# Performance work log

Hardware: AMD Instinct MI355X
Metric: run time of the kernel (lower is better)

Reference implementation:

```python
import jax, jax.numpy as jnp
import numpy as np

DECAY = 0.99
EPS = 1e-05


def setup_inputs() -> dict:
    key = jax.random.key(0)
    k1, k2 = jax.random.split(key)
    B, T, D, K = 16, 4096, 256, 1024
    z = jax.random.normal(k1, (B, T, D), dtype=jnp.float32)
    embedding = jax.random.normal(k2, (D, K), dtype=jnp.float32)
    cluster_size = jnp.zeros((K,), dtype=jnp.float32)
    embedding_mean = embedding.copy()  # torch init: embedding.clone()
    return {"z": z, "embedding": embedding, "cluster_size": cluster_size,
            "embedding_mean": embedding_mean}


def reference(z, embedding, cluster_size, embedding_mean):
    """Training-mode forward of CodebookEMA (proj=False).

    z:              [B, T, D]
    embedding:      [D, K] codebook buffer
    cluster_size:   [K]    EMA cluster counts
    embedding_mean: [D, K] EMA cluster sums
    Returns (z_q, commitment_loss, codebook_loss, code,
             new_embedding, new_cluster_size, new_embedding_mean).
    """
    B, T, D = z.shape
    K = embedding.shape[1]
    z_flat = z.reshape(B * T, D)

    # squared-distance quantization: ||z||^2 - 2 z.E + ||e||^2  -> [BT, K]
    dist = ((z_flat * z_flat).sum(1, keepdims=True)
            - 2.0 * (z_flat @ embedding)
            + (embedding * embedding).sum(0)[None, :])
    idx = jnp.argmin(dist, axis=1)              # [BT]
    code = idx.reshape(B, T)

    # EMA codebook update (no one-hot materialization; use segment sums)
    counts = jax.ops.segment_sum(jnp.ones_like(idx, dtype=z.dtype), idx,
                                 num_segments=K)               # [K]
    emb_sum = jax.ops.segment_sum(z_flat, idx, num_segments=K).T  # [D, K]
    new_cluster_size = cluster_size * DECAY + (1.0 - DECAY) * counts
    new_embedding_mean = embedding_mean * DECAY + (1.0 - DECAY) * emb_sum
    n = new_cluster_size.sum()
    cs_norm = (new_cluster_size + EPS) / (n + K * EPS) * n     # Laplace-smoothed
    new_embedding = new_embedding_mean / cs_norm[None, :]      # [D, K]

    # dequantize with the *updated* codebook (as in the torch control flow)
    z_q = new_embedding.T[code]                                # [B, T, D]

    commitment_loss = ((jax.lax.stop_gradient(z_q) - z) ** 2).mean(axis=(1, 2))
    codebook_loss = jnp.zeros((B,), dtype=z.dtype)
    z_q = z + jax.lax.stop_gradient(z_q - z)  # straight-through estimator
    return (z_q, commitment_loss, codebook_loss, code,
            new_embedding, new_cluster_size, new_embedding_mean)
```

## Files before the change

### kernel.cpp

```cpp
#include <hip/hip_runtime.h>
#include <cfloat>
#include <climits>
#include <cstdint>

#define B_ 16
#define T_ 4096
#define D_ 256
#define K_ 1024
#define BT_ 65536
#define DECAYF 0.99f
#define OMDECAYF 0.01f
#define EPSF 1e-5f
#define TAUGAP 0.125f
#define CHUNK 32
#define GROUP 16
#define RMARGIN 0.01f

typedef float f32x4 __attribute__((ext_vector_type(4)));
typedef _Float16 f16x8 __attribute__((ext_vector_type(8)));

__device__ __forceinline__ void gload16(const void* g, void* l) {
    __builtin_amdgcn_global_load_lds(
        (const __attribute__((address_space(1))) void*)g,
        (__attribute__((address_space(3))) void*)l, 16, 0, 0);
}

__global__ void k_prep(const float* __restrict__ z, const float* __restrict__ E,
                       _Float16* __restrict__ zf, _Float16* __restrict__ EfT,
                       float* __restrict__ enorm, double* __restrict__ enorm64,
                       int* __restrict__ counts, int* __restrict__ nflag,
                       float* __restrict__ out_closs, float* __restrict__ out_cbl,
                       float* __restrict__ emb_sum) {
    int b = blockIdx.x;
    if (b < 8192) {
        int base = (b * 256 + threadIdx.x) * 8;
        float4 v0 = *(const float4*)(z + base);
        float4 v1 = *(const float4*)(z + base + 4);
        f16x8 h;
        h[0] = (_Float16)v0.x; h[1] = (_Float16)v0.y;
        h[2] = (_Float16)v0.z; h[3] = (_Float16)v0.w;
        h[4] = (_Float16)v1.x; h[5] = (_Float16)v1.y;
        h[6] = (_Float16)v1.z; h[7] = (_Float16)v1.w;
        *(f16x8*)(zf + base) = h;
    } else {
        __shared__ double rd[256];
        int n = b - 8192, d = threadIdx.x;
        float v = E[(size_t)d * K_ + n];
        EfT[(size_t)n * 256 + d] = (_Float16)v;
        rd[d] = (double)v * (double)v;
        __syncthreads();
        for (int st = 128; st > 0; st >>= 1) {
            if (d < st) rd[d] += rd[d + st];
            __syncthreads();
        }
        if (d == 0) { enorm[n] = (float)rd[0]; enorm64[n] = rd[0]; }
        emb_sum[(size_t)n * 256 + d] = 0.f;
        if (n < 4) counts[n * 256 + d] = 0;
        if (n == 4) {
            if (d < 16) out_closs[d] = 0.f;
            else if (d < 32) out_cbl[d - 16] = 0.f;
            else if (d == 32) *nflag = 0;
        }
    }
}

__global__ __launch_bounds__(512, 2) void k_argmin_mfma(
    const _Float16* __restrict__ zf, const _Float16* __restrict__ EfT,
    const float* __restrict__ enorm, int* __restrict__ code,
    int* __restrict__ flags, int* __restrict__ nflag, int* __restrict__ counts) {
    __shared__ _Float16 Ab[2][128 * 32];
    __shared__ _Float16 Bb[2][256 * 32];
    __shared__ float mg_d1[512];
    __shared__ int   mg_i1[512];
    __shared__ float mg_d2[512];

    const int t = threadIdx.x;
    const int row0 = blockIdx.x * 128;
    const int l = t & 63, wid = t >> 6;
    const int wr = wid >> 2, wc = wid & 3;
    const int lr = l & 15, lk = l >> 4;

    const int arow = t >> 2,          ablk = (t & 3) ^ ((arow >> 1) & 3);
    const int brow0 = t >> 2,         bblk0 = (t & 3) ^ ((brow0 >> 1) & 3);
    const int brow1 = (t + 512) >> 2, bblk1 = ((t + 512) & 3) ^ ((brow1 >> 1) & 3);

#define STAGE(it_, buf_) do {                                                       \
        int nc_ = (it_) >> 3; int kb_ = ((it_) & 7) * 32;                            \
        gload16(zf + (size_t)(row0 + arow) * 256 + kb_ + ablk * 8,                   \
                &Ab[buf_][(t & ~63) * 8]);                                           \
        gload16(EfT + (size_t)(nc_ * 256 + brow0) * 256 + kb_ + bblk0 * 8,           \
                &Bb[buf_][(t & ~63) * 8]);                                           \
        gload16(EfT + (size_t)(nc_ * 256 + brow1) * 256 + kb_ + bblk1 * 8,           \
                &Bb[buf_][((t + 512) & ~63) * 8]);                                   \
    } while (0)

    STAGE(0, 0);

    float D1[4][4], D2[4][4];
    int   I1[4][4];
    #pragma unroll
    for (int m = 0; m < 4; ++m)
        #pragma unroll
        for (int r = 0; r < 4; ++r) {
            D1[m][r] = FLT_MAX; D2[m][r] = FLT_MAX; I1[m][r] = 0x7fffffff;
        }

    f32x4 acc[4][4];
    for (int it = 0; it < 32; ++it) {
        if ((it & 7) == 0) {
            #pragma unroll
            for (int m = 0; m < 4; ++m)
                #pragma unroll
                for (int n = 0; n < 4; ++n) acc[m][n] = (f32x4){0.f, 0.f, 0.f, 0.f};
        }
        __syncthreads();
        if (it + 1 < 32) STAGE(it + 1, (it + 1) & 1);
        const _Float16* Abuf = Ab[it & 1];
        const _Float16* Bbuf = Bb[it & 1];
        f16x8 a[4], b[4];
        #pragma unroll
        for (int m = 0; m < 4; ++m) {
            int row = wr * 64 + m * 16 + lr;
            a[m] = *(const f16x8*)&Abuf[row * 32 + ((lk ^ ((row >> 1) & 3)) * 8)];
        }
        #pragma unroll
        for (int n = 0; n < 4; ++n) {
            int nn = wc * 64 + n * 16 + lr;
            b[n] = *(const f16x8*)&Bbuf[nn * 32 + ((lk ^ ((nn >> 1) & 3)) * 8)];
        }
        #pragma unroll
        for (int m = 0; m < 4; ++m)
            #pragma unroll
            for (int n = 0; n < 4; ++n)
                acc[m][n] = __builtin_amdgcn_mfma_f32_16x16x32_f16(
                    a[m], b[n], acc[m][n], 0, 0, 0);

        if ((it & 7) == 7) {
            int nc = it >> 3;
            float en[4];
            #pragma unroll
            for (int n = 0; n < 4; ++n)
                en[n] = enorm[nc * 256 + wc * 64 + n * 16 + lr];
            #pragma unroll
            for (int m = 0; m < 4; ++m)
                #pragma unroll
                for (int r = 0; r < 4; ++r)
                    #pragma unroll
                    for (int n = 0; n < 4; ++n) {
                        float dist = en[n] - 2.0f * acc[m][n][r];
                        int cg = nc * 256 + wc * 64 + n * 16 + lr;
                        if (dist < D1[m][r]) {
                            D2[m][r] = D1[m][r]; D1[m][r] = dist; I1[m][r] = cg;
                        } else D2[m][r] = fminf(D2[m][r], dist);
                    }
        }
    }
#undef STAGE

    #pragma unroll
    for (int m = 0; m < 4; ++m)
        #pragma unroll
        for (int r = 0; r < 4; ++r) {
            float d1 = D1[m][r], d2 = D2[m][r];
            int i1 = I1[m][r];
            #pragma unroll
            for (int mask = 1; mask < 16; mask <<= 1) {
                float pd1 = __shfl_xor(d1, mask);
                int   pi1 = __shfl_xor(i1, mask);
                float pd2 = __shfl_xor(d2, mask);
                if (pd1 < d1 || (pd1 == d1 && pi1 < i1)) {
                    d2 = fminf(d1, pd2); d1 = pd1; i1 = pi1;
                } else d2 = fminf(d2, pd1);
            }
            if (lr == 0) {
                int row = wr * 64 + m * 16 + lk * 4 + r;
                mg_d1[row * 4 + wc] = d1;
                mg_i1[row * 4 + wc] = i1;
                mg_d2[row * 4 + wc] = d2;
            }
        }
    __syncthreads();
    if (t < 128) {
        float b1 = FLT_MAX, b2 = FLT_MAX;
        int bi = 0x7fffffff;
        #pragma unroll
        for (int c = 0; c < 4; ++c) {
            float pd1 = mg_d1[t * 4 + c];
            int   pi1 = mg_i1[t * 4 + c];
            float pd2 = mg_d2[t * 4 + c];
            if (pd1 < b1 || (pd1 == b1 && pi1 < bi)) {
                b2 = fminf(b1, pd2); b1 = pd1; bi = pi1;
            } else b2 = fminf(b2, pd1);
        }
        code[row0 + t] = bi;
        atomicAdd(&counts[bi], 1);
        if (b2 - b1 < TAUGAP) {
            int pos = atomicAdd(nflag, 1);
            flags[pos] = row0 + t;
        }
    }
}

__global__ __launch_bounds__(256) void k_fixup(
    const float* __restrict__ z, const float* __restrict__ E,
    const float* __restrict__ enorm, const double* __restrict__ enorm64,
    const int* __restrict__ nflag, const int* __restrict__ flags,
    int* __restrict__ code, int* __restrict__ counts) {
    __shared__ float  zrows[GROUP][256];
    __shared__ int    rowid[GROUP];
    __shared__ float  bw[GROUP][4];
    __shared__ float  bestAll[GROUP];
    __shared__ int    ccnt[GROUP];
    __shared__ int    cand[GROUP][16];
    __shared__ double cdist[GROUP][16];

    const int t = threadIdx.x, w = t >> 6, l = t & 63;
    const int n = *nflag;
    const int ngroups = (n + GROUP - 1) / GROUP;

    for (int g = blockIdx.x; g < ngroups; g += gridDim.x) {
        __syncthreads();
        if (t < GROUP) {
            int idx = g * GROUP + t;
            rowid[t] = (idx < n) ? flags[idx] : -1;
            ccnt[t] = 0;
        }
        __syncthreads();
        {
            int i = t >> 4, s = t & 15;
            int r = rowid[i];
            const float* src = z + (size_t)(r < 0 ? 0 : r) * D_ + s * 16;
            float4 a0 = *(const float4*)(src + 0);
            float4 a1 = *(const float4*)(src + 4);
            float4 a2 = *(const float4*)(src + 8);
            float4 a3 = *(const float4*)(src + 12);
            *(float4*)&zrows[i][s * 16 + 0]  = a0;
            *(float4*)&zrows[i][s * 16 + 4]  = a1;
            *(float4*)&zrows[i][s * 16 + 8]  = a2;
            *(float4*)&zrows[i][s * 16 + 12] = a3;
        }
        __syncthreads();

        float acc[GROUP][4];
        #pragma unroll
        for (int i = 0; i < GROUP; ++i) {
            acc[i][0] = 0.f; acc[i][1] = 0.f; acc[i][2] = 0.f; acc[i][3] = 0.f;
        }
        const float* Ecol = E + 4 * t;
        for (int d = 0; d < D_; ++d) {
            float4 ev = *(const float4*)(Ecol + (size_t)d * K_);
            #pragma unroll
            for (int i = 0; i < GROUP; ++i) {
                float zd = zrows[i][d];
                acc[i][0] = fmaf(zd, ev.x, acc[i][0]);
                acc[i][1] = fmaf(zd, ev.y, acc[i][1]);
                acc[i][2] = fmaf(zd, ev.z, acc[i][2]);
                acc[i][3] = fmaf(zd, ev.w, acc[i][3]);
            }
        }
        float en0 = enorm[4 * t], en1 = enorm[4 * t + 1];
        float en2 = enorm[4 * t + 2], en3 = enorm[4 * t + 3];
        #pragma unroll
        for (int i = 0; i < GROUP; ++i) {
            acc[i][0] = en0 - 2.f * acc[i][0];
            acc[i][1] = en1 - 2.f * acc[i][1];
            acc[i][2] = en2 - 2.f * acc[i][2];
            acc[i][3] = en3 - 2.f * acc[i][3];
        }
        #pragma unroll
        for (int i = 0; i < GROUP; ++i) {
            float b = fminf(fminf(acc[i][0], acc[i][1]), fminf(acc[i][2], acc[i][3]));
            #pragma unroll
            for (int m = 1; m < 64; m <<= 1) b = fminf(b, __shfl_xor(b, m));
            if (l == 0) bw[i][w] = b;
        }
        __syncthreads();
        if (t < GROUP)
            bestAll[t] = fminf(fminf(bw[t][0], bw[t][1]), fminf(bw[t][2], bw[t][3]));
        __syncthreads();
        #pragma unroll
        for (int i = 0; i < GROUP; ++i) {
            float thr = bestAll[i] + RMARGIN;
            #pragma unroll
            for (int j = 0; j < 4; ++j) {
                if (acc[i][j] <= thr) {
                    int slot = atomicAdd(&ccnt[i], 1);
                    if (slot < 16) cand[i][slot] = 4 * t + j;
                }
            }
        }
        __syncthreads();
        for (int p = w; p < GROUP * 16; p += 4) {
            int i = p >> 4, s = p & 15;
            int cn = ccnt[i];
            if (rowid[i] < 0 || cn < 2 || s >= (cn < 16 ? cn : 16)) continue;
            int c = cand[i][s];
            double dot = 0.0;
            #pragma unroll
            for (int q = 0; q < 4; ++q) {
                int d = l * 4 + q;
                dot = fma((double)zrows[i][d], (double)E[(size_t)d * K_ + c], dot);
            }
            #pragma unroll
            for (int m = 1; m < 64; m <<= 1) dot += __shfl_xor(dot, m);
            if (l == 0) cdist[i][s] = enorm64[c] - 2.0 * dot;
        }
        __syncthreads();
        if (t < GROUP) {
            int r = rowid[t];
            if (r >= 0) {
                int cn = ccnt[t]; if (cn > 16) cn = 16;
                int newc;
                if (cn <= 1) {
                    newc = cand[t][0];
                } else {
                    double bd = DBL_MAX; int bi = INT_MAX;
                    for (int s = 0; s < cn; ++s) {
                        double dv = cdist[t][s]; int ci = cand[t][s];
                        if (dv < bd || (dv == bd && ci < bi)) { bd = dv; bi = ci; }
                    }
                    newc = bi;
                }
                int oldc = code[r];
                if (newc != oldc) {
                    code[r] = newc;
                    atomicSub(&counts[oldc], 1);
                    atomicAdd(&counts[newc], 1);
                }
            }
        }
    }
}

__global__ void k_scan(const int* __restrict__ counts, const float* __restrict__ cs,
                       int* __restrict__ offsets, int* __restrict__ cursor,
                       float* __restrict__ out_newcs, float* __restrict__ csnorm,
                       int* __restrict__ work, int* __restrict__ nwork) {
    __shared__ int   s[K_];
    __shared__ int   c[K_];
    __shared__ float red[K_];
    int t = threadIdx.x;
    int v = counts[t];
    int nch = (v + CHUNK - 1) / CHUNK;
    s[t] = v;
    c[t] = nch;
    float ncs = cs[t] * DECAYF + OMDECAYF * (float)v;
    out_newcs[t] = ncs;
    red[t] = ncs;
    __syncthreads();
    for (int d = 1; d < K_; d <<= 1) {
        int x = (t >= d) ? s[t - d] : 0;
        int y = (t >= d) ? c[t - d] : 0;
        __syncthreads();
        s[t] += x; c[t] += y;
        __syncthreads();
    }
    offsets[t] = s[t] - v;
    cursor[t]  = s[t] - v;
    if (t == K_ - 1) { offsets[K_] = s[t]; *nwork = c[t]; }
    int wbase = c[t] - nch;
    for (int j = 0; j < nch; ++j) work[wbase + j] = (t << 16) | j;
    for (int st = 512; st > 0; st >>= 1) {
        if (t < st) red[t] += red[t + st];
        __syncthreads();
    }
    float nsum = red[0];
    csnorm[t] = (ncs + EPSF) / (nsum + (float)K_ * EPSF) * nsum;
}

__global__ void k_sortidx(const int* __restrict__ code, int* __restrict__ cursor,
                          int* __restrict__ sorted) {
    int r = blockIdx.x * 256 + threadIdx.x;
    int cc = code[r];
    int pos = atomicAdd(&cursor[cc], 1);
    sorted[pos] = r;
}

__global__ void k_segsum(const float* __restrict__ z, const int* __restrict__ sorted,
                         const int* __restrict__ offsets, const int* __restrict__ work,
                         const int* __restrict__ nwork, float* __restrict__ emb_sum) {
    int NW = *nwork;
    int d = threadIdx.x;
    for (int i = blockIdx.x; i < NW; i += gridDim.x) {
        int wk = work[i];
        int k = wk >> 16, j = wk & 0xffff;
        int beg = offsets[k] + j * CHUNK;
        int end = min(beg + CHUNK, offsets[k + 1]);
        float s = 0.f;
        int idx = beg;
        for (; idx + 4 <= end; idx += 4) {
            int r0 = sorted[idx], r1 = sorted[idx + 1];
            int r2 = sorted[idx + 2], r3 = sorted[idx + 3];
            float v0 = z[(size_t)r0 * D_ + d];
            float v1 = z[(size_t)r1 * D_ + d];
            float v2 = z[(size_t)r2 * D_ + d];
            float v3 = z[(size_t)r3 * D_ + d];
            s += (v0 + v1) + (v2 + v3);
        }
        for (; idx < end; ++idx) s += z[(size_t)sorted[idx] * D_ + d];
        atomicAdd(&emb_sum[(size_t)k * D_ + d], s);
    }
}

__global__ void k_emb(const float* __restrict__ EM, const float* __restrict__ emb_sum,
                      const float* __restrict__ csnorm,
                      float* __restrict__ out_newemb, float* __restrict__ out_newem,
                      float* __restrict__ newembT) {
    int tid = blockIdx.x * 256 + threadIdx.x;
    int k = tid >> 8, d = tid & 255;
    float em  = EM[(size_t)d * K_ + k];
    float nem = em * DECAYF + OMDECAYF * emb_sum[tid];
    float nq  = nem / csnorm[k];
    out_newem [(size_t)d * K_ + k] = nem;
    out_newemb[(size_t)d * K_ + k] = nq;
    newembT[tid] = nq;
}

__global__ __launch_bounds__(256) void k_gather(
    const float* __restrict__ z, const int* __restrict__ code,
    const float* __restrict__ newembT,
    float* __restrict__ out_zq, float* __restrict__ out_code,
    float* __restrict__ out_closs) {
    __shared__ double wsum[4];
    const int w = threadIdx.x >> 6, l = threadIdx.x & 63;
    const int base = blockIdx.x * 32 + w * 8;
    double acc = 0.0;
    #pragma unroll
    for (int it = 0; it < 2; ++it) {
        const int r0 = base + it * 4;
        int i0 = code[r0], i1 = code[r0 + 1], i2 = code[r0 + 2], i3 = code[r0 + 3];
        float4 z0 = *(const float4*)(z + (size_t)(r0    ) * D_ + l * 4);
        float4 z1 = *(const float4*)(z + (size_t)(r0 + 1) * D_ + l * 4);
        float4 z2 = *(const float4*)(z + (size_t)(r0 + 2) * D_ + l * 4);
        float4 z3 = *(const float4*)(z + (size_t)(r0 + 3) * D_ + l * 4);
        float4 e0 = *(const float4*)(newembT + (size_t)i0 * D_ + l * 4);
        float4 e1 = *(const float4*)(newembT + (size_t)i1 * D_ + l * 4);
        float4 e2 = *(const float4*)(newembT + (size_t)i2 * D_ + l * 4);
        float4 e3 = *(const float4*)(newembT + (size_t)i3 * D_ + l * 4);
        *(float4*)(out_zq + (size_t)(r0    ) * D_ + l * 4) = e0;
        *(float4*)(out_zq + (size_t)(r0 + 1) * D_ + l * 4) = e1;
        *(float4*)(out_zq + (size_t)(r0 + 2) * D_ + l * 4) = e2;
        *(float4*)(out_zq + (size_t)(r0 + 3) * D_ + l * 4) = e3;
        if (l < 4) out_code[r0 + l] = (float)(l == 0 ? i0 : l == 1 ? i1 : l == 2 ? i2 : i3);
        float dx, dy, dz2, dw2;
        dx = e0.x - z0.x; dy = e0.y - z0.y; dz2 = e0.z - z0.z; dw2 = e0.w - z0.w;
        acc += (double)dx * dx + (double)dy * dy + (double)dz2 * dz2 + (double)dw2 * dw2;
        dx = e1.x - z1.x; dy = e1.y - z1.y; dz2 = e1.z - z1.z; dw2 = e1.w - z1.w;
        acc += (double)dx * dx + (double)dy * dy + (double)dz2 * dz2 + (double)dw2 * dw2;
        dx = e2.x - z2.x; dy = e2.y - z2.y; dz2 = e2.z - z2.z; dw2 = e2.w - z2.w;
        acc += (double)dx * dx + (double)dy * dy + (double)dz2 * dz2 + (double)dw2 * dw2;
        dx = e3.x - z3.x; dy = e3.y - z3.y; dz2 = e3.z - z3.z; dw2 = e3.w - z3.w;
        acc += (double)dx * dx + (double)dy * dy + (double)dz2 * dz2 + (double)dw2 * dw2;
    }
    #pragma unroll
    for (int off = 32; off > 0; off >>= 1) acc += __shfl_down(acc, off);
    if (l == 0) wsum[w] = acc;
    __syncthreads();
    if (threadIdx.x == 0) {
        float v = (float)((wsum[0] + wsum[1] + wsum[2] + wsum[3]) *
                          (1.0 / ((double)T_ * (double)D_)));
        atomicAdd(&out_closs[blockIdx.x >> 7], v);
    }
}

extern "C" void kernel_launch(void* const* d_in, const int* in_sizes, int n_in,
                              void* d_out, int out_size, void* d_ws, size_t ws_size,
                              hipStream_t stream) {
    (void)in_sizes; (void)n_in; (void)out_size; (void)ws_size;
    const float* z  = (const float*)d_in[0];
    const float* E  = (const float*)d_in[1];
    const float* cs = (const float*)d_in[2];
    const float* EM = (const float*)d_in[3];

    float* out       = (float*)d_out;
    float* out_zq    = out;
    float* out_closs = out + 16777216;
    float* out_cbl   = out_closs + 16;
    float* out_code  = out_cbl + 16;
    float* out_nemb  = out_code + 65536;
    float* out_ncs   = out_nemb + 262144;
    float* out_nem   = out_ncs + 1024;

    _Float16* zf = (_Float16*)out_zq;

    char* w = (char*)d_ws;
    int*      counts  = (int*)(w + 0);
    int*      nflag   = (int*)(w + 4096);
    int*      offsets = (int*)(w + 4160);
    int*      cursor  = (int*)(w + 8320);
    float*    enorm   = (float*)(w + 12416);
    int*      code_i  = (int*)(w + 16512);
    int*      flags   = (int*)(w + 278656);
    float*    csnorm  = (float*)(w + 540800);
    float*    newembT = (float*)(w + 544896);
    _Float16* EfT     = (_Float16*)(w + 1593472);
    int*      sorted  = (int*)(w + 2117760);
    float*    emb_sum = (float*)(w + 2379904);
    int*      work    = (int*)(w + 3428480);
    int*      nwork   = (int*)(w + 3444864);
    double*   enorm64 = (double*)(w + 3444928);

    k_prep       <<<9216, 256, 0, stream>>>(z, E, zf, EfT, enorm, enorm64, counts,
                                            nflag, out_closs, out_cbl, emb_sum);
    k_argmin_mfma<<<BT_ / 128, 512, 0, stream>>>(zf, EfT, enorm, code_i, flags,
                                                 nflag, counts);
    k_fixup      <<<256, 256, 0, stream>>>(z, E, enorm, enorm64, nflag, flags,
                                           code_i, counts);
    k_scan       <<<1, K_, 0, stream>>>(counts, cs, offsets, cursor, out_ncs, csnorm,
                                        work, nwork);
    k_sortidx    <<<BT_ / 256, 256, 0, stream>>>(code_i, cursor, sorted);
    k_segsum     <<<2048, 256, 0, stream>>>(z, sorted, offsets, work, nwork, emb_sum);
    k_emb        <<<(K_ * D_) / 256, 256, 0, stream>>>(EM, emb_sum, csnorm,
                                                       out_nemb, out_nem, newembT);
    k_gather     <<<BT_ / 32, 256, 0, stream>>>(z, code_i, newembT, out_zq, out_code,
                                                out_closs);
}
```

Baseline: 291.2 us.

## Raise argmin occupancy, reuse LDS for merge, unroll segsum and gather loads

The argmin kernel's launch bounds move from 2 to 6 waves-per-EU hint, and its merge scratch arrays now alias the A tile buffer after a barrier instead of taking extra LDS. Both changes aim to fit more blocks per CU. The segment-sum inner loop is unrolled to 8 rows to put more loads in flight. The gather kernel issues all 8 rows' loads up front rather than in two batches. The tighter register budget risks spills in the MFMA argmin kernel, and the gather and segsum unrolls raise register pressure.

```diff
diff --git a/kernel.cpp b/kernel.cpp
--- a/kernel.cpp
+++ b/kernel.cpp
@@ -64,15 +64,12 @@
     }
 }
 
-__global__ __launch_bounds__(512, 2) void k_argmin_mfma(
+__global__ __launch_bounds__(512, 6) void k_argmin_mfma(
     const _Float16* __restrict__ zf, const _Float16* __restrict__ EfT,
     const float* __restrict__ enorm, int* __restrict__ code,
     int* __restrict__ flags, int* __restrict__ nflag, int* __restrict__ counts) {
     __shared__ _Float16 Ab[2][128 * 32];
     __shared__ _Float16 Bb[2][256 * 32];
-    __shared__ float mg_d1[512];
-    __shared__ int   mg_i1[512];
-    __shared__ float mg_d2[512];
 
     const int t = threadIdx.x;
     const int row0 = blockIdx.x * 128;
@@ -156,6 +153,11 @@
         }
     }
 #undef STAGE
+
+    __syncthreads();
+    float* mg_d1 = (float*)&Ab[0][0];
+    int*   mg_i1 = (int*)(mg_d1 + 512);
+    float* mg_d2 = (float*)(mg_i1 + 512);
 
     #pragma unroll
     for (int m = 0; m < 4; ++m)
@@ -388,14 +390,20 @@
         int end = min(beg + CHUNK, offsets[k + 1]);
         float s = 0.f;
         int idx = beg;
-        for (; idx + 4 <= end; idx += 4) {
-            int r0 = sorted[idx], r1 = sorted[idx + 1];
+        for (; idx + 8 <= end; idx += 8) {
+            int r0 = sorted[idx],     r1 = sorted[idx + 1];
             int r2 = sorted[idx + 2], r3 = sorted[idx + 3];
+            int r4 = sorted[idx + 4], r5 = sorted[idx + 5];
+            int r6 = sorted[idx + 6], r7 = sorted[idx + 7];
             float v0 = z[(size_t)r0 * D_ + d];
             float v1 = z[(size_t)r1 * D_ + d];
             float v2 = z[(size_t)r2 * D_ + d];
             float v3 = z[(size_t)r3 * D_ + d];
-            s += (v0 + v1) + (v2 + v3);
+            float v4 = z[(size_t)r4 * D_ + d];
+            float v5 = z[(size_t)r5 * D_ + d];
+            float v6 = z[(size_t)r6 * D_ + d];
+            float v7 = z[(size_t)r7 * D_ + d];
+            s += ((v0 + v1) + (v2 + v3)) + ((v4 + v5) + (v6 + v7));
         }
         for (; idx < end; ++idx) s += z[(size_t)sorted[idx] * D_ + d];
         atomicAdd(&emb_sum[(size_t)k * D_ + d], s);
@@ -424,34 +432,56 @@
     __shared__ double wsum[4];
     const int w = threadIdx.x >> 6, l = threadIdx.x & 63;
     const int base = blockIdx.x * 32 + w * 8;
+    int i0 = code[base],     i1 = code[base + 1], i2 = code[base + 2], i3 = code[base + 3];
+    int i4 = code[base + 4], i5 = code[base + 5], i6 = code[base + 6], i7 = code[base + 7];
+    float4 z0 = *(const float4*)(z + (size_t)(base    ) * D_ + l * 4);
+    float4 z1 = *(const float4*)(z + (size_t)(base + 1) * D_ + l * 4);
+    float4 z2 = *(const float4*)(z + (size_t)(base + 2) * D_ + l * 4);
+    float4 z3 = *(const float4*)(z + (size_t)(base + 3) * D_ + l * 4);
+    float4 z4 = *(const float4*)(z + (size_t)(base + 4) * D_ + l * 4);
+    float4 z5 = *(const float4*)(z + (size_t)(base + 5) * D_ + l * 4);
+    float4 z6 = *(const float4*)(z + (size_t)(base + 6) * D_ + l * 4);
+    float4 z7 = *(const float4*)(z + (size_t)(base + 7) * D_ + l * 4);
+    float4 e0 = *(const float4*)(newembT + (size_t)i0 * D_ + l * 4);
+    float4 e1 = *(const float4*)(newembT + (size_t)i1 * D_ + l * 4);
+    float4 e2 = *(const float4*)(newembT + (size_t)i2 * D_ + l * 4);
+    float4 e3 = *(const float4*)(newembT + (size_t)i3 * D_ + l * 4);
+    float4 e4 = *(const float4*)(newembT + (size_t)i4 * D_ + l * 4);
+    float4 e5 = *(const float4*)(newembT + (size_t)i5 * D_ + l * 4);
+    float4 e6 = *(const float4*)(newembT + (size_t)i6 * D_ + l * 4);
+    float4 e7 = *(const float4*)(newembT + (size_t)i7 * D_ + l * 4);
+    *(float4*)(out_zq + (size_t)(base    ) * D_ + l * 4) = e0;
+    *(float4*)(out_zq + (size_t)(base + 1) * D_ + l * 4) = e1;
+    *(float4*)(out_zq + (size_t)(base + 2) * D_ + l * 4) = e2;
+    *(float4*)(out_zq + (size_t)(base + 3) * D_ + l * 4) = e3;
+    *(float4*)(out_zq + (size_t)(base + 4) * D_ + l * 4) = e4;
+    *(float4*)(out_zq + (size_t)(base + 5) * D_ + l * 4) = e5;
+    *(float4*)(out_zq + (size_t)(base + 6) * D_ + l * 4) = e6;
+    *(float4*)(out_zq + (size_t)(base + 7) * D_ + l * 4) = e7;
+    if (l == 0) {
+        out_code[base]     = (float)i0; out_code[base + 1] = (float)i1;
+        out_code[base + 2] = (float)i2; out_code[base + 3] = (float)i3;
+        out_code[base + 4] = (float)i4; out_code[base + 5] = (float)i5;
+        out_code[base + 6] = (float)i6; out_code[base + 7] = (float)i7;
+    }
     double acc = 0.0;
-    #pragma unroll
-    for (int it = 0; it < 2; ++it) {
-        const int r0 = base + it * 4;
-        int i0 = code[r0], i1 = code[r0 + 1], i2 = code[r0 + 2], i3 = code[r0 + 3];
-        float4 z0 = *(const float4*)(z + (size_t)(r0    ) * D_ + l * 4);
-        float4 z1 = *(const float4*)(z + (size_t)(r0 + 1) * D_ + l * 4);
-        float4 z2 = *(const float4*)(z + (size_t)(r0 + 2) * D_ + l * 4);
-        float4 z3 = *(const float4*)(z + (size_t)(r0 + 3) * D_ + l * 4);
-        float4 e0 = *(const float4*)(newembT + (size_t)i0 * D_ + l * 4);
-        float4 e1 = *(const float4*)(newembT + (size_t)i1 * D_ + l * 4);
-        float4 e2 = *(const float4*)(newembT + (size_t)i2 * D_ + l * 4);
-        float4 e3 = *(const float4*)(newembT + (size_t)i3 * D_ + l * 4);
-        *(float4*)(out_zq + (size_t)(r0    ) * D_ + l * 4) = e0;
-        *(float4*)(out_zq + (size_t)(r0 + 1) * D_ + l * 4) = e1;
-        *(float4*)(out_zq + (size_t)(r0 + 2) * D_ + l * 4) = e2;
-        *(float4*)(out_zq + (size_t)(r0 + 3) * D_ + l * 4) = e3;
-        if (l < 4) out_code[r0 + l] = (float)(l == 0 ? i0 : l == 1 ? i1 : l == 2 ? i2 : i3);
-        float dx, dy, dz2, dw2;
-        dx = e0.x - z0.x; dy = e0.y - z0.y; dz2 = e0.z - z0.z; dw2 = e0.w - z0.w;
-        acc += (double)dx * dx + (double)dy * dy + (double)dz2 * dz2 + (double)dw2 * dw2;
-        dx = e1.x - z1.x; dy = e1.y - z1.y; dz2 = e1.z - z1.z; dw2 = e1.w - z1.w;
-        acc += (double)dx * dx + (double)dy * dy + (double)dz2 * dz2 + (double)dw2 * dw2;
-        dx = e2.x - z2.x; dy = e2.y - z2.y; dz2 = e2.z - z2.z; dw2 = e2.w - z2.w;
-        acc += (double)dx * dx + (double)dy * dy + (double)dz2 * dz2 + (double)dw2 * dw2;
-        dx = e3.x - z3.x; dy = e3.y - z3.y; dz2 = e3.z - z3.z; dw2 = e3.w - z3.w;
-        acc += (double)dx * dx + (double)dy * dy + (double)dz2 * dz2 + (double)dw2 * dw2;
-    }
+    float dx, dy, dz2, dw2;
+    dx = e0.x - z0.x; dy = e0.y - z0.y; dz2 = e0.z - z0.z; dw2 = e0.w - z0.w;
+    acc += (double)dx * dx + (double)dy * dy + (double)dz2 * dz2 + (double)dw2 * dw2;
+    dx = e1.x - z1.x; dy = e1.y - z1.y; dz2 = e1.z - z1.z; dw2 = e1.w - z1.w;
+    acc += (double)dx * dx + (double)dy * dy + (double)dz2 * dz2 + (double)dw2 * dw2;
+    dx = e2.x - z2.x; dy = e2.y - z2.y; dz2 = e2.z - z2.z; dw2 = e2.w - z2.w;
+    acc += (double)dx * dx + (double)dy * dy + (double)dz2 * dz2 + (double)dw2 * dw2;
+    dx = e3.x - z3.x; dy = e3.y - z3.y; dz2 = e3.z - z3.z; dw2 = e3.w - z3.w;
+    acc += (double)dx * dx + (double)dy * dy + (double)dz2 * dz2 + (double)dw2 * dw2;
+    dx = e4.x - z4.x; dy = e4.y - z4.y; dz2 = e4.z - z4.z; dw2 = e4.w - z4.w;
+    acc += (double)dx * dx + (double)dy * dy + (double)dz2 * dz2 + (double)dw2 * dw2;
+    dx = e5.x - z5.x; dy = e5.y - z5.y; dz2 = e5.z - z5.z; dw2 = e5.w - z5.w;
+    acc += (double)dx * dx + (double)dy * dy + (double)dz2 * dz2 + (double)dw2 * dw2;
+    dx = e6.x - z6.x; dy = e6.y - z6.y; dz2 = e6.z - z6.z; dw2 = e6.w - z6.w;
+    acc += (double)dx * dx + (double)dy * dy + (double)dz2 * dz2 + (double)dw2 * dw2;
+    dx = e7.x - z7.x; dy = e7.y - z7.y; dz2 = e7.z - z7.z; dw2 = e7.w - z7.w;
+    acc += (double)dx * dx + (double)dy * dy + (double)dz2 * dz2 + (double)dw2 * dw2;
     #pragma unroll
     for (int off = 32; off > 0; off >>= 1) acc += __shfl_down(acc, off);
     if (l == 0) wsum[w] = acc;
```

Result: slower. 490.6 us (+68.5%).
